# Kernel tuning notes

Hardware: AMD Instinct MI355X
Metric: run time of the kernel (lower is better)

The kernel has to match this reference:

```python
import jax, jax.numpy as jnp
import numpy as np

STRIDE = 8
PAD = 8
KSZ = 16


def setup_inputs() -> dict:
    key = jax.random.key(0)
    k1, k2, k3 = jax.random.split(key, 3)
    B, Cin, Cout, L = 16, 512, 1, 4000
    inp = jax.random.normal(k1, (B, Cin, L), dtype=jnp.float32)
    # t60 in [0.1, 0.5) so that round(t60*100)-10 lands in [0, 40]
    t60s = 0.1 + 0.39 * jax.random.uniform(k2, (B // 2,), dtype=jnp.float32)
    kernel_weight = jax.random.uniform(k3, (41, Cin, Cout, KSZ), dtype=jnp.float32)
    return {"input": inp, "t60s": t60s, "kernel_weight": kernel_weight}


def reference(input, t60s, kernel_weight):
    # per-sample kernel index: round(t60*100).int().repeat(2) - 10
    idx = jnp.tile(jnp.round(t60s * 100.0).astype(jnp.int32), 2) - 10  # (B,)
    w = kernel_weight[idx]                      # (B, Cin, Cout, K) gathered per sample
    # torch conv_transpose1d(x, W) == conv(x with lhs_dilation=stride,
    #                                      flip_k(W).swap(Cin,Cout), pad=K-1-p)
    w = jnp.flip(jnp.swapaxes(w, 1, 2), axis=-1)  # (B, Cout, Cin, K)
    pad = KSZ - 1 - PAD

    def per_sample(x, wk):  # x: (Cin, L), wk: (Cout, Cin, K)
        y = jax.lax.conv_general_dilated(
            x[None], wk,
            window_strides=(1,),
            padding=[(pad, pad)],
            lhs_dilation=(STRIDE,),
            dimension_numbers=("NCH", "OIH", "NCH"),
        )
        return y[0]  # (Cout, L_out), L_out = (L-1)*stride - 2*PAD + K

    return jax.vmap(per_sample)(input, w)  # (B, Cout, L_out)
```

## Files before the change

kernel.cpp:

```cpp
#include <hip/hip_runtime.h>

#define L_IN   4000
#define CIN    512
#define KSZ    16
#define LOUT   31992
#define NQ     3999
#define QTILE  64

__global__ __launch_bounds__(256, 4)
void dereverb_kernel(const float* __restrict__ x,
                     const float* __restrict__ t60s,
                     const float* __restrict__ kw,
                     float* __restrict__ out)
{
    __shared__ float lds[CIN * KSZ];

    const int b    = blockIdx.y;
    const int q0   = blockIdx.x * QTILE;
    const int tid  = threadIdx.x;
    const int lane = tid & 63;
    const int wave = tid >> 6;

    float t60 = t60s[b & 7];
    int kidx = (int)rintf(t60 * 100.0f) - 10;
    kidx = __builtin_amdgcn_readfirstlane(kidx);
    const float4* wsrc = (const float4*)(kw + (size_t)kidx * (CIN * KSZ));

    #pragma unroll
    for (int i = 0; i < 8; ++i)
        ((float4*)lds)[tid + i * 256] = wsrc[tid + i * 256];
    __syncthreads();

    const int q  = q0 + lane;
    const int qc = q < (NQ - 1) ? q : (NQ - 1);

    const int cw = wave * 128;
    const float*  xp = x + ((size_t)b * CIN + cw) * L_IN + qc;
    const float4* wl = (const float4*)(lds + cw * KSZ);

    float acc[8];
    #pragma unroll
    for (int r = 0; r < 8; ++r) acc[r] = 0.0f;

    #pragma unroll 8
    for (int i = 0; i < 128; ++i) {
        float x0 = xp[0];
        float x1 = xp[1];
        float4 wv[4];
        wv[0] = wl[0];
        wv[1] = wl[1];
        wv[2] = wl[2];
        wv[3] = wl[3];
        const float* wf = (const float*)wv;
        #pragma unroll
        for (int r = 0; r < 8; ++r) {
            acc[r] = fmaf(x1, wf[r],     acc[r]);
            acc[r] = fmaf(x0, wf[r + 8], acc[r]);
        }
        xp += L_IN;
        wl += 4;
    }

    if (q > NQ - 1) {
        #pragma unroll
        for (int r = 0; r < 8; ++r) acc[r] = 0.0f;
    }

    __syncthreads();
    float* red = lds;
    #pragma unroll
    for (int r = 0; r < 8; ++r)
        red[wave * 520 + r * 65 + lane] = acc[r];
    __syncthreads();

    const int base_t = q0 * 8;
    const int j0 = tid * 2;
    if (base_t + j0 < LOUT) {
        float s0 = 0.0f, s1 = 0.0f;
        #pragma unroll
        for (int w = 0; w < 4; ++w) {
            s0 += red[w * 520 + ((j0)     & 7) * 65 + ((j0)     >> 3)];
            s1 += red[w * 520 + ((j0 + 1) & 7) * 65 + ((j0 + 1) >> 3)];
        }
        *(float2*)(out + (size_t)b * LOUT + base_t + j0) = make_float2(s0, s1);
    }
}

extern "C" void kernel_launch(void* const* d_in, const int* in_sizes, int n_in,
                              void* d_out, int out_size, void* d_ws, size_t ws_size,
                              hipStream_t stream) {
    const float* x    = (const float*)d_in[0];
    const float* t60s = (const float*)d_in[1];
    const float* kw   = (const float*)d_in[2];
    float* out = (float*)d_out;

    dim3 grid((NQ + QTILE - 1) / QTILE, 16);
    dereverb_kernel<<<grid, 256, 0, stream>>>(x, t60s, kw, out);
}
```

Baseline: 190.4 us.

## Process four q-columns per thread with 8 waves splitting channels

Each thread now accumulates four output position groups (256 q per block) so every LDS weight load is reused across four columns, and 8 waves each cover 64 input channels. The cross-wave reduction moves to a padded stride-9 LDS layout summed over 8 waves. This cuts LDS weight traffic per FMA and the number of blocks, but it reduces the grid to 256 blocks and raises register pressure, which may lower occupancy and memory-level parallelism.

```diff
diff --git a/kernel.cpp b/kernel.cpp
--- a/kernel.cpp
+++ b/kernel.cpp
@@ -1,22 +1,23 @@
 #include <hip/hip_runtime.h>
 
-#define L_IN   4000
-#define CIN    512
-#define KSZ    16
-#define LOUT   31992
-#define NQ     3999
-#define QTILE  64
+#define L_IN    4000
+#define CIN     512
+#define KSZ     16
+#define LOUT    31992
+#define NQ      3999
+#define QPB     256
+#define RSTRIDE 2304
 
-__global__ __launch_bounds__(256, 4)
+__global__ __launch_bounds__(512, 2)
 void dereverb_kernel(const float* __restrict__ x,
                      const float* __restrict__ t60s,
                      const float* __restrict__ kw,
                      float* __restrict__ out)
 {
-    __shared__ float lds[CIN * KSZ];
+    __shared__ float lds[8 * RSTRIDE];
 
     const int b    = blockIdx.y;
-    const int q0   = blockIdx.x * QTILE;
+    const int q0   = blockIdx.x * QPB;
     const int tid  = threadIdx.x;
     const int lane = tid & 63;
     const int wave = tid >> 6;
@@ -27,62 +28,80 @@
     const float4* wsrc = (const float4*)(kw + (size_t)kidx * (CIN * KSZ));
 
     #pragma unroll
-    for (int i = 0; i < 8; ++i)
-        ((float4*)lds)[tid + i * 256] = wsrc[tid + i * 256];
+    for (int i = 0; i < 4; ++i)
+        ((float4*)lds)[tid + i * 512] = wsrc[tid + i * 512];
     __syncthreads();
 
-    const int q  = q0 + lane;
-    const int qc = q < (NQ - 1) ? q : (NQ - 1);
+    const float* xb = x + ((size_t)b * CIN + wave * 64) * L_IN;
+    const float* xp[4];
+    #pragma unroll
+    for (int qi = 0; qi < 4; ++qi) {
+        int q  = q0 + qi * 64 + lane;
+        int qc = q < NQ - 1 ? q : (NQ - 1);
+        xp[qi] = xb + qc;
+    }
 
-    const int cw = wave * 128;
-    const float*  xp = x + ((size_t)b * CIN + cw) * L_IN + qc;
-    const float4* wl = (const float4*)(lds + cw * KSZ);
+    const float4* wl = (const float4*)(lds + wave * 64 * KSZ);
 
-    float acc[8];
+    float acc[4][8];
     #pragma unroll
-    for (int r = 0; r < 8; ++r) acc[r] = 0.0f;
+    for (int qi = 0; qi < 4; ++qi)
+        #pragma unroll
+        for (int r = 0; r < 8; ++r) acc[qi][r] = 0.0f;
 
-    #pragma unroll 8
-    for (int i = 0; i < 128; ++i) {
-        float x0 = xp[0];
-        float x1 = xp[1];
+    #pragma unroll 2
+    for (int ci = 0; ci < 64; ++ci) {
+        float x0[4], x1[4];
+        #pragma unroll
+        for (int qi = 0; qi < 4; ++qi) {
+            x0[qi] = xp[qi][0];
+            x1[qi] = xp[qi][1];
+            xp[qi] += L_IN;
+        }
         float4 wv[4];
         wv[0] = wl[0];
         wv[1] = wl[1];
         wv[2] = wl[2];
         wv[3] = wl[3];
+        wl += 4;
         const float* wf = (const float*)wv;
         #pragma unroll
-        for (int r = 0; r < 8; ++r) {
-            acc[r] = fmaf(x1, wf[r],     acc[r]);
-            acc[r] = fmaf(x0, wf[r + 8], acc[r]);
-        }
-        xp += L_IN;
-        wl += 4;
+        for (int qi = 0; qi < 4; ++qi)
+            #pragma unroll
+            for (int r = 0; r < 8; ++r) {
+                acc[qi][r] = fmaf(x1[qi], wf[r],     acc[qi][r]);
+                acc[qi][r] = fmaf(x0[qi], wf[r + 8], acc[qi][r]);
+            }
     }
 
-    if (q > NQ - 1) {
-        #pragma unroll
-        for (int r = 0; r < 8; ++r) acc[r] = 0.0f;
-    }
+    #pragma unroll
+    for (int qi = 0; qi < 4; ++qi)
+        if (q0 + qi * 64 + lane > NQ - 1)
+            #pragma unroll
+            for (int r = 0; r < 8; ++r) acc[qi][r] = 0.0f;
 
     __syncthreads();
-    float* red = lds;
     #pragma unroll
-    for (int r = 0; r < 8; ++r)
-        red[wave * 520 + r * 65 + lane] = acc[r];
+    for (int qi = 0; qi < 4; ++qi) {
+        int ql = qi * 64 + lane;
+        float* rp = lds + wave * RSTRIDE + 9 * ql;
+        #pragma unroll
+        for (int r = 0; r < 8; ++r) rp[r] = acc[qi][r];
+    }
     __syncthreads();
 
-    const int base_t = q0 * 8;
-    const int j0 = tid * 2;
-    if (base_t + j0 < LOUT) {
-        float s0 = 0.0f, s1 = 0.0f;
-        #pragma unroll
-        for (int w = 0; w < 4; ++w) {
-            s0 += red[w * 520 + ((j0)     & 7) * 65 + ((j0)     >> 3)];
-            s1 += red[w * 520 + ((j0 + 1) & 7) * 65 + ((j0 + 1) >> 3)];
+    const size_t ob = (size_t)b * LOUT + (size_t)q0 * 8;
+    #pragma unroll
+    for (int k = 0; k < 4; ++k) {
+        int tl = k * 512 + tid;
+        if (q0 * 8 + tl < LOUT) {
+            int ql = tl >> 3, r = tl & 7;
+            float s = 0.0f;
+            #pragma unroll
+            for (int w = 0; w < 8; ++w)
+                s += lds[w * RSTRIDE + 9 * ql + r];
+            out[ob + tl] = s;
         }
-        *(float2*)(out + (size_t)b * LOUT + base_t + j0) = make_float2(s0, s1);
     }
 }
 
@@ -94,6 +113,6 @@
     const float* kw   = (const float*)d_in[2];
     float* out = (float*)d_out;
 
-    dim3 grid((NQ + QTILE - 1) / QTILE, 16);
-    dereverb_kernel<<<grid, 256, 0, stream>>>(x, t60s, kw, out);
+    dim3 grid((NQ + QPB - 1) / QPB, 16);
+    dereverb_kernel<<<grid, 512, 0, stream>>>(x, t60s, kw, out);
 }
```

Result: no change. 190.9 us (+0.2%).
